# Kernel tuning notes

Hardware: AMD Instinct MI355X
Metric: run time of the kernel (lower is better)

Reference implementation:

```python
import jax, jax.numpy as jnp
import numpy as np

N_HEAD = 16


def setup_inputs() -> dict:
    key = jax.random.key(0)
    ks = jax.random.split(key, 5)
    B, T, C = 4, 2048, 1024
    s = 0.02
    return {
        "x": jax.random.normal(ks[0], (B, T, C), dtype=jnp.float32),
        "Wq": jax.random.normal(ks[1], (C, C), dtype=jnp.float32) * s,
        "Wk": jax.random.normal(ks[2], (C, C), dtype=jnp.float32) * s,
        "Wv": jax.random.normal(ks[3], (C, C), dtype=jnp.float32) * s,
        "Wp": jax.random.normal(ks[4], (C, C), dtype=jnp.float32) * s,
    }


def reference(x, Wq, Wk, Wv, Wp):
    B, T, C = x.shape
    H = N_HEAD
    D = C // H
    # torch Linear(bias=False): x @ W.T
    q = (x @ Wq.T).reshape(B, T, H, D).transpose(0, 2, 1, 3)  # [B,H,T,D]
    k = (x @ Wk.T).reshape(B, T, H, D).transpose(0, 2, 1, 3)
    v = (x @ Wv.T).reshape(B, T, H, D).transpose(0, 2, 1, 3)
    scale = 1.0 / jnp.sqrt(jnp.float32(D))
    att = jnp.einsum("bhqd,bhkd->bhqk", q, k) * scale  # [B,H,T,T]
    causal = jnp.tril(jnp.ones((T, T), dtype=bool))
    att = jnp.where(causal, att, jnp.float32(-jnp.inf))
    att = jax.nn.softmax(att, axis=-1)
    y = jnp.einsum("bhqk,bhkd->bhqd", att, v)  # [B,H,T,D]
    y = y.transpose(0, 2, 1, 3).reshape(B, T, C)
    return y @ Wp.T
```

## Files before the change

kernel.cpp:

```cpp
#include <hip/hip_runtime.h>
#include <hip/hip_bf16.h>
#include <math.h>

typedef __hip_bfloat16 bf16;
typedef __attribute__((ext_vector_type(8))) short short8;
typedef __attribute__((ext_vector_type(4))) float f32x4;
typedef __attribute__((ext_vector_type(2))) unsigned uint2v;
typedef __attribute__((ext_vector_type(4))) unsigned uint4v;

#define MFMA_BF16(a, b, c) __builtin_amdgcn_mfma_f32_16x16x32_bf16((a), (b), (c), 0, 0, 0)

__device__ __forceinline__ void async_copy16(const bf16* g, bf16* l) {
  __builtin_amdgcn_global_load_lds(
      (const __attribute__((address_space(1))) void*)g,
      (__attribute__((address_space(3))) void*)l,
      16, 0, 0);
}

__device__ __forceinline__ unsigned short f2bf_bits(float f) {
  bf16 h = __float2bfloat16(f);
  return *reinterpret_cast<unsigned short*>(&h);
}

__device__ __forceinline__ unsigned cvt_pk_bf16(float lo, float hi) {
  unsigned r;
  asm("v_cvt_pk_bf16_f32 %0, %1, %2" : "=v"(r) : "v"(lo), "v"(hi));
  return r;
}

__global__ __launch_bounds__(256) void cvt_all(const float* __restrict__ x,
                                               const float* __restrict__ wq,
                                               const float* __restrict__ wk,
                                               const float* __restrict__ wv,
                                               const float* __restrict__ wp,
                                               bf16* __restrict__ xb, bf16* __restrict__ wqb,
                                               bf16* __restrict__ wkb, bf16* __restrict__ wvb,
                                               bf16* __restrict__ wpb) {
  const int bid = blockIdx.x;
  const float* in;
  bf16* out;
  int off;
  float scale = 1.0f;
  if (bid < 8192) {
    in = x; out = xb; off = bid;
  } else if (bid < 9216) {
    in = wq; out = wqb; off = bid - 8192;
    scale = 0.180336880111112f;
  } else if (bid < 10240) {
    in = wk; out = wkb; off = bid - 9216;
  } else if (bid < 11264) {
    in = wv; out = wvb; off = bid - 10240;
  } else {
    in = wp; out = wpb; off = bid - 11264;
  }
  const int i = off * 256 + threadIdx.x;
  float4 v = reinterpret_cast<const float4*>(in)[i];
  ushort4 u;
  u.x = f2bf_bits(v.x * scale);
  u.y = f2bf_bits(v.y * scale);
  u.z = f2bf_bits(v.z * scale);
  u.w = f2bf_bits(v.w * scale);
  reinterpret_cast<ushort4*>(out)[i] = u;
}

__device__ __forceinline__ void gemm_core256(const bf16* __restrict__ A,
                                             const bf16* __restrict__ W,
                                             f32x4 (&acc)[4][4]) {
  __shared__ __align__(16) bf16 L[4][12288];
  const int t = threadIdx.x;
  const int lane = t & 63;
  const int l15 = lane & 15;
  const int quad = (lane >> 4) & 3;
  const int wave = t >> 6;
  const int wm = (wave >> 1) * 64;
  const int wn = (wave & 1) * 64;
  const int K = 1024;

  const f32x4 zero = {0.f, 0.f, 0.f, 0.f};
#pragma unroll
  for (int m = 0; m < 4; ++m)
#pragma unroll
    for (int n = 0; n < 4; ++n) acc[m][n] = zero;

  const int srow = t >> 2;
  const int schunk = ((t & 3) ^ ((t >> 3) & 3)) * 8;
  const bf16* ga0 = A + (size_t)(blockIdx.y * 256 + srow) * K + schunk;
  const bf16* ga1 = ga0 + (size_t)128 * K;
  const bf16* gb0 = W + (size_t)(blockIdx.x * 128 + srow) * K + schunk;

  const int fsw = (quad ^ ((l15 >> 1) & 3)) * 8;
  const int arow = (wm + l15) * 32 + fsw;
  const int brow = 8192 + (wn + l15) * 32 + fsw;

#pragma unroll
  for (int kt = 0; kt < 3; ++kt) {
    bf16* Ld = &L[kt][0];
    async_copy16(ga0 + kt * 32, Ld + t * 8);
    async_copy16(ga1 + kt * 32, Ld + 4096 + t * 8);
    async_copy16(gb0 + kt * 32, Ld + 8192 + t * 8);
  }
  asm volatile("s_waitcnt vmcnt(6)" ::: "memory");
  __builtin_amdgcn_s_barrier();

  for (int T = 0; T < 32; ++T) {
    const bf16* Lb = &L[T & 3][0];
    short8 af[4], bfr[4];
#pragma unroll
    for (int m = 0; m < 4; ++m)
      af[m] = *reinterpret_cast<const short8*>(Lb + arow + m * 512);
#pragma unroll
    for (int n = 0; n < 4; ++n)
      bfr[n] = *reinterpret_cast<const short8*>(Lb + brow + n * 512);
    if (T <= 28) {
      bf16* Ld = &L[(T + 3) & 3][0];
      async_copy16(ga0 + (T + 3) * 32, Ld + t * 8);
      async_copy16(ga1 + (T + 3) * 32, Ld + 4096 + t * 8);
      async_copy16(gb0 + (T + 3) * 32, Ld + 8192 + t * 8);
    }
    if (T < 29)
      asm volatile("s_waitcnt vmcnt(6)" ::: "memory");
    else if (T == 29)
      asm volatile("s_waitcnt vmcnt(3)" ::: "memory");
    else
      asm volatile("s_waitcnt vmcnt(0)" ::: "memory");
    __builtin_amdgcn_s_barrier();
    asm volatile("s_waitcnt lgkmcnt(0)" ::: "memory");
    __builtin_amdgcn_sched_barrier(0);
    __builtin_amdgcn_s_setprio(1);
#pragma unroll
    for (int m = 0; m < 4; ++m)
#pragma unroll
      for (int n = 0; n < 4; ++n) acc[m][n] = MFMA_BF16(af[m], bfr[n], acc[m][n]);
    __builtin_amdgcn_s_setprio(0);
    __builtin_amdgcn_sched_barrier(0);
    __builtin_amdgcn_s_barrier();
  }
}

__global__ __launch_bounds__(512, 2) void gemm_qkv(const bf16* __restrict__ x,
                                                   const bf16* __restrict__ wq,
                                                   const bf16* __restrict__ wk,
                                                   const bf16* __restrict__ wv,
                                                   bf16* __restrict__ q, bf16* __restrict__ k,
                                                   bf16* __restrict__ vt) {
  const bf16* W = (blockIdx.z == 0) ? wq : (blockIdx.z == 1) ? wk : wv;
  f32x4 acc[4][4];
  gemm_core256(x, W, acc);
  const int t = threadIdx.x, lane = t & 63, l15 = lane & 15, quad = (lane >> 4) & 3,
            wave = t >> 6;
  const int wm = (wave >> 1) * 64, wn = (wave & 1) * 64;
  const int rb = blockIdx.y * 256 + wm + quad * 4;
  const int cbb = blockIdx.x * 128 + wn + l15;
  if (blockIdx.z == 2) {
#pragma unroll
    for (int m = 0; m < 4; ++m)
#pragma unroll
      for (int n = 0; n < 4; ++n) {
        const int tg = rb + m * 16;
        const int col = cbb + n * 16;
        const int b = tg >> 11, tl = tg & 2047;
        const int tls = (tl & ~12) | ((tl & 4) << 1) | ((tl & 8) >> 1);
        ushort4 pk;
        pk.x = f2bf_bits(acc[m][n][0]);
        pk.y = f2bf_bits(acc[m][n][1]);
        pk.z = f2bf_bits(acc[m][n][2]);
        pk.w = f2bf_bits(acc[m][n][3]);
        *reinterpret_cast<ushort4*>(&vt[((size_t)(b * 1024 + col)) * 2048 + tls]) = pk;
      }
  } else {
    bf16* C = (blockIdx.z == 0) ? q : k;
#pragma unroll
    for (int m = 0; m < 4; ++m)
#pragma unroll
      for (int n = 0; n < 4; ++n)
#pragma unroll
        for (int r = 0; r < 4; ++r)
          C[(size_t)(rb + m * 16 + r) * 1024 + cbb + n * 16] = __float2bfloat16(acc[m][n][r]);
  }
}

__global__ __launch_bounds__(512, 2) void gemm_proj(const bf16* __restrict__ y,
                                                    const bf16* __restrict__ wp,
                                                    float* __restrict__ outp) {
  f32x4 acc[4][4];
  gemm_core256(y, wp, acc);
  const int t = threadIdx.x, lane = t & 63, l15 = lane & 15, quad = (lane >> 4) & 3,
            wave = t >> 6;
  const int wm = (wave >> 1) * 64, wn = (wave & 1) * 64;
  const int rb = blockIdx.y * 256 + wm + quad * 4;
  const int cbb = blockIdx.x * 128 + wn + l15;
#pragma unroll
  for (int m = 0; m < 4; ++m)
#pragma unroll
    for (int n = 0; n < 4; ++n)
#pragma unroll
      for (int r = 0; r < 4; ++r)
        outp[(size_t)(rb + m * 16 + r) * 1024 + cbb + n * 16] = acc[m][n][r];
}

__global__ __launch_bounds__(256) void attn(const bf16* __restrict__ qb,
                                            const bf16* __restrict__ kb,
                                            const bf16* __restrict__ vt,
                                            bf16* __restrict__ yb) {
  __shared__ __align__(16) bf16 Ks[2][2048];
  __shared__ __align__(16) bf16 Vs[2][2048];
  const int tid = threadIdx.x;
  const int lane = tid & 63, l15 = lane & 15, quad = lane >> 4, wave = tid >> 6;
  const int p = blockIdx.y;
  const int bh = blockIdx.x;
  const int b = bh >> 4, h = bh & 15;
  const size_t rowbase = (size_t)b * 2048;
  const int cb = h * 64;

  const int tlo = p, thi = 31 - p;
  const int gq0[2] = {tlo * 64 + wave * 16, thi * 64 + wave * 16};

  short8 aq[2][2];
#pragma unroll
  for (int g = 0; g < 2; ++g) {
    const bf16* qp = qb + (rowbase + gq0[g] + l15) * 1024 + cb + quad * 8;
    aq[g][0] = *reinterpret_cast<const short8*>(qp);
    aq[g][1] = *reinterpret_cast<const short8*>(qp + 32);
  }

  short8 ones;
#pragma unroll
  for (int i = 0; i < 8; ++i) ones[i] = (short)0x3F80;

  f32x4 o[2][4], l4[2];
  const f32x4 zero = {0.f, 0.f, 0.f, 0.f};
#pragma unroll
  for (int g = 0; g < 2; ++g) {
#pragma unroll
    for (int dt = 0; dt < 4; ++dt) o[g][dt] = zero;
    l4[g] = zero;
  }

  const int sdq = (((tid & 3) ^ ((tid >> 2) & 3) ^ ((tid >> 4) & 3))) * 8;
  const bf16* kg = kb + (rowbase + ((tid & 127) >> 2)) * 1024 + cb + (tid >> 7) * 32 + sdq;
  const bf16* vg = vt + ((size_t)bh * 64 + (tid >> 2)) * 2048 + sdq;
  const int csw = (quad ^ (l15 & 3) ^ ((l15 >> 2) & 3)) * 8;

  const int nkt = 2 * thi + 2;
  async_copy16(kg, &Ks[0][tid * 8]);
  async_copy16(vg, &Vs[0][tid * 8]);

  for (int kt = 0; kt < nkt; ++kt) {
    const int buf = kt & 1;
    __syncthreads();
    if (kt + 1 < nkt) {
      async_copy16(kg + (size_t)(kt + 1) * 32 * 1024, &Ks[buf ^ 1][tid * 8]);
      async_copy16(vg + (kt + 1) * 32, &Vs[buf ^ 1][tid * 8]);
    }
    const int k0g = kt * 32;
    if (k0g > gq0[1] + 15) continue;

    short8 bk[2][2];
#pragma unroll
    for (int j = 0; j < 2; ++j)
#pragma unroll
      for (int ks = 0; ks < 2; ++ks)
        bk[j][ks] = *reinterpret_cast<const short8*>(
            &Ks[buf][ks * 1024 + (j * 16 + l15) * 32 + csw]);
    short8 av[4];
#pragma unroll
    for (int dt = 0; dt < 4; ++dt)
      av[dt] = *reinterpret_cast<const short8*>(&Vs[buf][(dt * 16 + l15) * 32 + csw]);

#pragma unroll
    for (int g = 0; g < 2; ++g) {
      if (k0g > gq0[g] + 15) continue;
      f32x4 st[2];
#pragma unroll
      for (int j = 0; j < 2; ++j) {
        st[j] = MFMA_BF16(bk[j][0], aq[g][0], zero);
        st[j] = MFMA_BF16(bk[j][1], aq[g][1], st[j]);
      }
      const bool need_mask = (k0g + 31 > gq0[g]);
      unsigned w[2][2];
#pragma unroll
      for (int j = 0; j < 2; ++j) {
        float pw[4];
#pragma unroll
        for (int r = 0; r < 4; ++r) {
          float val = st[j][r];
          if (need_mask && (k0g + j * 16 + quad * 4 + r) > (gq0[g] + l15))
            val = -INFINITY;
          pw[r] = __builtin_amdgcn_exp2f(val);
        }
        w[j][0] = cvt_pk_bf16(pw[0], pw[1]);
        w[j][1] = cvt_pk_bf16(pw[2], pw[3]);
      }
      uint2v s0 = __builtin_amdgcn_permlane32_swap(w[0][0], w[1][0], false, false);
      uint2v s1 = __builtin_amdgcn_permlane32_swap(w[0][1], w[1][1], false, false);
      uint4v u;
      u[0] = s0[0];
      u[1] = s1[0];
      u[2] = s0[1];
      u[3] = s1[1];
      const short8 bp = __builtin_bit_cast(short8, u);
#pragma unroll
      for (int dt = 0; dt < 4; ++dt) o[g][dt] = MFMA_BF16(av[dt], bp, o[g][dt]);
      l4[g] = MFMA_BF16(ones, bp, l4[g]);
    }
  }

#pragma unroll
  for (int g = 0; g < 2; ++g) {
    const float invl = 1.f / l4[g][0];
    bf16* yp = yb + (rowbase + gq0[g] + l15) * 1024 + cb + quad * 4;
#pragma unroll
    for (int dt = 0; dt < 4; ++dt) {
      ushort4 pk;
      pk.x = f2bf_bits(o[g][dt][0] * invl);
      pk.y = f2bf_bits(o[g][dt][1] * invl);
      pk.z = f2bf_bits(o[g][dt][2] * invl);
      pk.w = f2bf_bits(o[g][dt][3] * invl);
      *reinterpret_cast<ushort4*>(&yp[dt * 16]) = pk;
    }
  }
}

extern "C" void kernel_launch(void* const* d_in, const int* in_sizes, int n_in,
                              void* d_out, int out_size, void* d_ws, size_t ws_size,
                              hipStream_t stream) {
  const float* x = (const float*)d_in[0];
  const float* Wq = (const float*)d_in[1];
  const float* Wk = (const float*)d_in[2];
  const float* Wv = (const float*)d_in[3];
  const float* Wp = (const float*)d_in[4];
  float* out = (float*)d_out;

  const size_t MB = 1024 * 1024;
  char* ws = (char*)d_ws;
  bf16* xb = (bf16*)(ws);
  bf16* qb = (bf16*)(ws + 16 * MB);
  bf16* kb = (bf16*)(ws + 32 * MB);
  bf16* vtb = (bf16*)(ws + 48 * MB);
  bf16* wqb = (bf16*)(ws + 64 * MB);
  bf16* wkb = (bf16*)(ws + 66 * MB);
  bf16* wvb = (bf16*)(ws + 68 * MB);
  bf16* wpb = (bf16*)(ws + 70 * MB);
  bf16* yb = xb;

  cvt_all<<<12288, 256, 0, stream>>>(x, Wq, Wk, Wv, Wp, xb, wqb, wkb, wvb, wpb);
  gemm_qkv<<<dim3(8, 32, 3), 512, 0, stream>>>(xb, wqb, wkb, wvb, qb, kb, vtb);
  attn<<<dim3(64, 16), 256, 0, stream>>>(qb, kb, vtb, yb);
  gemm_proj<<<dim3(8, 32), 512, 0, stream>>>(yb, wpb, out);
}
```

Baseline: 277.8 us.

## Fuse Q/K/V GEMMs into one block sharing A tiles, add XCD-aware tile mapping

The QKV GEMM now has each block compute all three projections for the same 256x128 tile, so the x tile loaded into LDS is reused three times instead of being reloaded by three separate blocks. The pipeline drops from four to three LDS stages with a prefetch depth of two to fit the larger per-stage footprint. A block-index remapping spreads tiles across XCDs for better L2 locality, and it also applies to the projection GEMM. The cost is triple the accumulator registers (48 f32x4 per thread), which risks spills or lower occupancy under launch_bounds(512,2), plus less prefetch depth.

```diff
diff --git a/kernel.cpp b/kernel.cpp
--- a/kernel.cpp
+++ b/kernel.cpp
@@ -63,10 +63,14 @@
   reinterpret_cast<ushort4*>(out)[i] = u;
 }
 
-__device__ __forceinline__ void gemm_core256(const bf16* __restrict__ A,
-                                             const bf16* __restrict__ W,
-                                             f32x4 (&acc)[4][4]) {
-  __shared__ __align__(16) bf16 L[4][12288];
+template <int NZ>
+__device__ __forceinline__ void gemm_fused_core(const bf16* __restrict__ A,
+                                                const bf16* __restrict__ w0,
+                                                const bf16* __restrict__ w1,
+                                                const bf16* __restrict__ w2,
+                                                int bx, int by,
+                                                f32x4 (&acc)[NZ][4][4]) {
+  __shared__ __align__(16) bf16 L[3][8192 + NZ * 4096];
   const int t = threadIdx.x;
   const int lane = t & 63;
   const int l15 = lane & 15;
@@ -78,63 +82,82 @@
 
   const f32x4 zero = {0.f, 0.f, 0.f, 0.f};
 #pragma unroll
-  for (int m = 0; m < 4; ++m)
-#pragma unroll
-    for (int n = 0; n < 4; ++n) acc[m][n] = zero;
+  for (int z = 0; z < NZ; ++z)
+#pragma unroll
+    for (int m = 0; m < 4; ++m)
+#pragma unroll
+      for (int n = 0; n < 4; ++n) acc[z][m][n] = zero;
 
   const int srow = t >> 2;
   const int schunk = ((t & 3) ^ ((t >> 3) & 3)) * 8;
-  const bf16* ga0 = A + (size_t)(blockIdx.y * 256 + srow) * K + schunk;
+  const bf16* ga0 = A + (size_t)(by * 256 + srow) * K + schunk;
   const bf16* ga1 = ga0 + (size_t)128 * K;
-  const bf16* gb0 = W + (size_t)(blockIdx.x * 128 + srow) * K + schunk;
+  const bf16* ws[3] = {w0, w1, w2};
+  const bf16* gw[NZ];
+#pragma unroll
+  for (int z = 0; z < NZ; ++z)
+    gw[z] = ws[z] + (size_t)(bx * 128 + srow) * K + schunk;
 
   const int fsw = (quad ^ ((l15 >> 1) & 3)) * 8;
   const int arow = (wm + l15) * 32 + fsw;
-  const int brow = 8192 + (wn + l15) * 32 + fsw;
-
-#pragma unroll
-  for (int kt = 0; kt < 3; ++kt) {
-    bf16* Ld = &L[kt][0];
+  const int brow = (wn + l15) * 32 + fsw;
+
+  auto stage = [&](int kt) {
+    bf16* Ld = &L[kt % 3][0];
     async_copy16(ga0 + kt * 32, Ld + t * 8);
     async_copy16(ga1 + kt * 32, Ld + 4096 + t * 8);
-    async_copy16(gb0 + kt * 32, Ld + 8192 + t * 8);
-  }
-  asm volatile("s_waitcnt vmcnt(6)" ::: "memory");
+#pragma unroll
+    for (int z = 0; z < NZ; ++z)
+      async_copy16(gw[z] + kt * 32, Ld + 8192 + z * 4096 + t * 8);
+  };
+
+  stage(0);
+  stage(1);
+  if constexpr (NZ == 3)
+    asm volatile("s_waitcnt vmcnt(5)" ::: "memory");
+  else
+    asm volatile("s_waitcnt vmcnt(3)" ::: "memory");
   __builtin_amdgcn_s_barrier();
 
   for (int T = 0; T < 32; ++T) {
-    const bf16* Lb = &L[T & 3][0];
-    short8 af[4], bfr[4];
+    const bf16* Lb = &L[T % 3][0];
+    short8 af[4];
 #pragma unroll
     for (int m = 0; m < 4; ++m)
       af[m] = *reinterpret_cast<const short8*>(Lb + arow + m * 512);
-#pragma unroll
-    for (int n = 0; n < 4; ++n)
-      bfr[n] = *reinterpret_cast<const short8*>(Lb + brow + n * 512);
-    if (T <= 28) {
-      bf16* Ld = &L[(T + 3) & 3][0];
-      async_copy16(ga0 + (T + 3) * 32, Ld + t * 8);
-      async_copy16(ga1 + (T + 3) * 32, Ld + 4096 + t * 8);
-      async_copy16(gb0 + (T + 3) * 32, Ld + 8192 + t * 8);
-    }
-    if (T < 29)
-      asm volatile("s_waitcnt vmcnt(6)" ::: "memory");
-    else if (T == 29)
-      asm volatile("s_waitcnt vmcnt(3)" ::: "memory");
-    else
+    if (T <= 29) {
+      stage(T + 2);
+      if constexpr (NZ == 3)
+        asm volatile("s_waitcnt vmcnt(5)" ::: "memory");
+      else
+        asm volatile("s_waitcnt vmcnt(3)" ::: "memory");
+    } else {
       asm volatile("s_waitcnt vmcnt(0)" ::: "memory");
+    }
     __builtin_amdgcn_s_barrier();
     asm volatile("s_waitcnt lgkmcnt(0)" ::: "memory");
     __builtin_amdgcn_sched_barrier(0);
     __builtin_amdgcn_s_setprio(1);
 #pragma unroll
-    for (int m = 0; m < 4; ++m)
-#pragma unroll
-      for (int n = 0; n < 4; ++n) acc[m][n] = MFMA_BF16(af[m], bfr[n], acc[m][n]);
+    for (int z = 0; z < NZ; ++z) {
+      short8 bfr[4];
+#pragma unroll
+      for (int n = 0; n < 4; ++n)
+        bfr[n] = *reinterpret_cast<const short8*>(Lb + 8192 + z * 4096 + brow + n * 512);
+#pragma unroll
+      for (int m = 0; m < 4; ++m)
+#pragma unroll
+        for (int n = 0; n < 4; ++n) acc[z][m][n] = MFMA_BF16(af[m], bfr[n], acc[z][m][n]);
+    }
     __builtin_amdgcn_s_setprio(0);
     __builtin_amdgcn_sched_barrier(0);
     __builtin_amdgcn_s_barrier();
   }
+}
+
+__device__ __forceinline__ void xcd_map(int i, int& bx, int& by) {
+  bx = (i >> 3) & 7;
+  by = (i & 7) * 4 + (i >> 6);
 }
 
 __global__ __launch_bounds__(512, 2) void gemm_qkv(const bf16* __restrict__ x,
@@ -143,59 +166,62 @@
                                                    const bf16* __restrict__ wv,
                                                    bf16* __restrict__ q, bf16* __restrict__ k,
                                                    bf16* __restrict__ vt) {
-  const bf16* W = (blockIdx.z == 0) ? wq : (blockIdx.z == 1) ? wk : wv;
-  f32x4 acc[4][4];
-  gemm_core256(x, W, acc);
+  int bx, by;
+  xcd_map(blockIdx.x, bx, by);
+  f32x4 acc[3][4][4];
+  gemm_fused_core<3>(x, wq, wk, wv, bx, by, acc);
   const int t = threadIdx.x, lane = t & 63, l15 = lane & 15, quad = (lane >> 4) & 3,
             wave = t >> 6;
   const int wm = (wave >> 1) * 64, wn = (wave & 1) * 64;
-  const int rb = blockIdx.y * 256 + wm + quad * 4;
-  const int cbb = blockIdx.x * 128 + wn + l15;
-  if (blockIdx.z == 2) {
+  const int rb = by * 256 + wm + quad * 4;
+  const int cbb = bx * 128 + wn + l15;
+#pragma unroll
+  for (int z = 0; z < 2; ++z) {
+    bf16* C = z ? k : q;
 #pragma unroll
     for (int m = 0; m < 4; ++m)
 #pragma unroll
-      for (int n = 0; n < 4; ++n) {
-        const int tg = rb + m * 16;
-        const int col = cbb + n * 16;
-        const int b = tg >> 11, tl = tg & 2047;
-        const int tls = (tl & ~12) | ((tl & 4) << 1) | ((tl & 8) >> 1);
-        ushort4 pk;
-        pk.x = f2bf_bits(acc[m][n][0]);
-        pk.y = f2bf_bits(acc[m][n][1]);
-        pk.z = f2bf_bits(acc[m][n][2]);
-        pk.w = f2bf_bits(acc[m][n][3]);
-        *reinterpret_cast<ushort4*>(&vt[((size_t)(b * 1024 + col)) * 2048 + tls]) = pk;
-      }
-  } else {
-    bf16* C = (blockIdx.z == 0) ? q : k;
-#pragma unroll
-    for (int m = 0; m < 4; ++m)
-#pragma unroll
       for (int n = 0; n < 4; ++n)
 #pragma unroll
         for (int r = 0; r < 4; ++r)
-          C[(size_t)(rb + m * 16 + r) * 1024 + cbb + n * 16] = __float2bfloat16(acc[m][n][r]);
-  }
+          C[(size_t)(rb + m * 16 + r) * 1024 + cbb + n * 16] = __float2bfloat16(acc[z][m][n][r]);
+  }
+#pragma unroll
+  for (int m = 0; m < 4; ++m)
+#pragma unroll
+    for (int n = 0; n < 4; ++n) {
+      const int tg = rb + m * 16;
+      const int col = cbb + n * 16;
+      const int b = tg >> 11, tl = tg & 2047;
+      const int tls = (tl & ~12) | ((tl & 4) << 1) | ((tl & 8) >> 1);
+      ushort4 pk;
+      pk.x = f2bf_bits(acc[2][m][n][0]);
+      pk.y = f2bf_bits(acc[2][m][n][1]);
+      pk.z = f2bf_bits(acc[2][m][n][2]);
+      pk.w = f2bf_bits(acc[2][m][n][3]);
+      *reinterpret_cast<ushort4*>(&vt[((size_t)(b * 1024 + col)) * 2048 + tls]) = pk;
+    }
 }
 
 __global__ __launch_bounds__(512, 2) void gemm_proj(const bf16* __restrict__ y,
                                                     const bf16* __restrict__ wp,
                                                     float* __restrict__ outp) {
-  f32x4 acc[4][4];
-  gemm_core256(y, wp, acc);
+  int bx, by;
+  xcd_map(blockIdx.x, bx, by);
+  f32x4 acc[1][4][4];
+  gemm_fused_core<1>(y, wp, wp, wp, bx, by, acc);
   const int t = threadIdx.x, lane = t & 63, l15 = lane & 15, quad = (lane >> 4) & 3,
             wave = t >> 6;
   const int wm = (wave >> 1) * 64, wn = (wave & 1) * 64;
-  const int rb = blockIdx.y * 256 + wm + quad * 4;
-  const int cbb = blockIdx.x * 128 + wn + l15;
+  const int rb = by * 256 + wm + quad * 4;
+  const int cbb = bx * 128 + wn + l15;
 #pragma unroll
   for (int m = 0; m < 4; ++m)
 #pragma unroll
     for (int n = 0; n < 4; ++n)
 #pragma unroll
       for (int r = 0; r < 4; ++r)
-        outp[(size_t)(rb + m * 16 + r) * 1024 + cbb + n * 16] = acc[m][n][r];
+        outp[(size_t)(rb + m * 16 + r) * 1024 + cbb + n * 16] = acc[0][m][n][r];
 }
 
 __global__ __launch_bounds__(256) void attn(const bf16* __restrict__ qb,
@@ -344,7 +370,7 @@
   bf16* yb = xb;
 
   cvt_all<<<12288, 256, 0, stream>>>(x, Wq, Wk, Wv, Wp, xb, wqb, wkb, wvb, wpb);
-  gemm_qkv<<<dim3(8, 32, 3), 512, 0, stream>>>(xb, wqb, wkb, wvb, qb, kb, vtb);
+  gemm_qkv<<<256, 512, 0, stream>>>(xb, wqb, wkb, wvb, qb, kb, vtb);
   attn<<<dim3(64, 16), 256, 0, stream>>>(qb, kb, vtb, yb);
-  gemm_proj<<<dim3(8, 32), 512, 0, stream>>>(yb, wpb, out);
-}
+  gemm_proj<<<256, 512, 0, stream>>>(yb, wpb, out);
+}
```

New measurement: 258.7 us. 6.9% less time.
